# Kernel tuning notes

Measured on AMD Instinct MI355X. Metric: run time of the kernel, lower is better.

## Reference

```python
import jax, jax.numpy as jnp
import numpy as np

N_NODES = 100000
N_EDGES = 1600000
DIMS = [64, 64, 64, 32]  # [n_feat] + hid


def setup_inputs() -> dict:
    key = jax.random.key(0)
    ks = jax.random.split(key, 2 + 2 * (len(DIMS) - 1))
    x = jax.random.normal(ks[0], (N_NODES, DIMS[0]), dtype=jnp.float32)
    edge_index = jax.random.randint(ks[1], (2, N_EDGES), 0, N_NODES, dtype=jnp.int64)
    inp = {"x": x, "edge_index": edge_index}
    for i in range(len(DIMS) - 1):
        fan_in, fan_out = DIMS[i], DIMS[i + 1]
        scale = 1.0 / np.sqrt(fan_in)
        inp[f"W{i+1}"] = jax.random.normal(ks[2 + 2 * i], (fan_in, fan_out), dtype=jnp.float32) * scale
        inp[f"b{i+1}"] = jax.random.normal(ks[3 + 2 * i], (fan_out,), dtype=jnp.float32) * scale
    return inp


def _gcn_conv(x, W, b, src, dst, dis):
    # h = X W ; out[i] = sum_{j->i} norm_ij * h[j] + dis[i]^2 * h[i] + b
    h = x @ W
    norm = dis[src] * dis[dst]                      # [E]
    agg = jax.ops.segment_sum(h[src] * norm[:, None], dst, num_segments=x.shape[0])
    agg = agg + h * (dis * dis)[:, None]            # self-loop contribution
    return agg + b


def reference(x, edge_index, W1, b1, W2, b2, W3, b3):
    src, dst = edge_index[0], edge_index[1]
    n = x.shape[0]
    # degree with self-loops (edge weight 1), symmetric normalization
    deg = jax.ops.segment_sum(jnp.ones(src.shape[0], x.dtype), dst, num_segments=n) + 1.0
    dis = jax.lax.rsqrt(deg)
    h = jax.nn.relu(_gcn_conv(x, W1, b1, src, dst, dis))   # dropout is identity in eval
    h = jax.nn.relu(_gcn_conv(h, W2, b2, src, dst, dis))
    return _gcn_conv(h, W3, b3, src, dst, dis)
```

## Files before the change

kernel.cpp:

```cpp
#include <hip/hip_runtime.h>


typedef __attribute__((ext_vector_type(8))) _Float16 half8;

static inline int cdiv(int a, int b) { return (a + b - 1) / b; }

#define ACHUNK 4096
#define MAXNBK 512

__global__ void k_bucket_hist(const int* __restrict__ dst, int* __restrict__ counts_t,
                              int NBK, int NBA, int E) {
    __shared__ int cnt[MAXNBK];
    int t = threadIdx.x, b = blockIdx.x;
    for (int i = t; i < NBK; i += 256) cnt[i] = 0;
    __syncthreads();
    int e0 = b * ACHUNK;
#pragma unroll
    for (int j = 0; j < ACHUNK / 256; ++j) {
        int e = e0 + j * 256 + t;
        if (e < E) atomicAdd(&cnt[dst[e] >> 8], 1);
    }
    __syncthreads();
    for (int i = t; i < NBK; i += 256) counts_t[i * NBA + b] = cnt[i];
}

#define SCAN_T 256
#define SCAN_V 4
#define SCAN_CHUNK 1024

__global__ void k_scan_partial(const int* __restrict__ a, int* __restrict__ bsum, int n) {
    __shared__ int red[SCAN_T];
    int t = threadIdx.x, b = blockIdx.x;
    int base = b * SCAN_CHUNK + t * SCAN_V;
    int s = 0;
#pragma unroll
    for (int j = 0; j < SCAN_V; ++j) { int i = base + j; if (i < n) s += a[i]; }
    red[t] = s;
    __syncthreads();
    for (int off = SCAN_T / 2; off > 0; off >>= 1) {
        if (t < off) red[t] += red[t + off];
        __syncthreads();
    }
    if (t == 0) bsum[b] = red[0];
}

__global__ void k_scan_bsum(int* bsum, int nb) {
    __shared__ int sh[1024];
    int t = threadIdx.x;
    int v = (t < nb) ? bsum[t] : 0;
    sh[t] = v;
    __syncthreads();
    for (int off = 1; off < 1024; off <<= 1) {
        int u = (t >= off) ? sh[t - off] : 0;
        __syncthreads();
        sh[t] += u;
        __syncthreads();
    }
    if (t < nb) bsum[t] = sh[t] - v;
}

__global__ void k_scan_final(const int* __restrict__ a, const int* __restrict__ bsum,
                             int* __restrict__ out, int n) {
    __shared__ int sh[SCAN_T];
    int t = threadIdx.x, b = blockIdx.x;
    int base = b * SCAN_CHUNK + t * SCAN_V;
    int v[SCAN_V];
    int s = 0;
#pragma unroll
    for (int j = 0; j < SCAN_V; ++j) {
        int i = base + j;
        v[j] = (i < n) ? a[i] : 0;
        s += v[j];
    }
    sh[t] = s;
    __syncthreads();
    for (int off = 1; off < SCAN_T; off <<= 1) {
        int u = (t >= off) ? sh[t - off] : 0;
        __syncthreads();
        sh[t] += u;
        __syncthreads();
    }
    int run = sh[t] - s + bsum[b];
#pragma unroll
    for (int j = 0; j < SCAN_V; ++j) {
        int i = base + j;
        if (i < n) { out[i] = run; run += v[j]; }
    }
}

__global__ void k_bucket_scatter(const int* __restrict__ src, const int* __restrict__ dst,
                                 const int* __restrict__ offsets, unsigned* __restrict__ bucketed,
                                 int NBK, int NBA, int E) {
    __shared__ int curs[MAXNBK];
    int t = threadIdx.x, b = blockIdx.x;
    for (int i = t; i < NBK; i += 256) curs[i] = offsets[i * NBA + b];
    __syncthreads();
    int e0 = b * ACHUNK;
#pragma unroll
    for (int j = 0; j < ACHUNK / 256; ++j) {
        int e = e0 + j * 256 + t;
        if (e < E) {
            int d = dst[e];
            int pos = atomicAdd(&curs[d >> 8], 1);
            bucketed[pos] = (unsigned)src[e] | ((unsigned)(d & 255) << 24);
        }
    }
}

__global__ void k_bucket_build(const unsigned* __restrict__ bucketed,
                               const int* __restrict__ offsets,
                               int* __restrict__ csr_src, int* __restrict__ row_start,
                               float* __restrict__ dis, int NBK, int NBA, int N, int E) {
    __shared__ int cnt[256];
    __shared__ int sc[256];
    int t = threadIdx.x, k = blockIdx.x;
    int base = offsets[k * NBA];
    int end = (k + 1 < NBK) ? offsets[(k + 1) * NBA] : E;
    cnt[t] = 0;
    __syncthreads();
    for (int i = base + t; i < end; i += 256)
        atomicAdd(&cnt[bucketed[i] >> 24], 1);
    __syncthreads();
    int c = cnt[t];
    sc[t] = c;
    __syncthreads();
    for (int off = 1; off < 256; off <<= 1) {
        int u = (t >= off) ? sc[t - off] : 0;
        __syncthreads();
        sc[t] += u;
        __syncthreads();
    }
    int excl = sc[t] - c;
    int node = k * 256 + t;
    if (node < N) {
        row_start[node] = base + excl;
        dis[node] = rsqrtf(1.0f + (float)c);
    }
    if (k == 0 && t == 0) row_start[N] = E;
    cnt[t] = base + excl;
    __syncthreads();
    for (int i = base + t; i < end; i += 256) {
        unsigned w = bucketed[i];
        int pos = atomicAdd(&cnt[w >> 24], 1);
        csr_src[pos] = (int)(w & 0xFFFFFFu);
    }
}

template <int K, int M>
__global__ void k_gemm(const float* __restrict__ X, const float* __restrict__ W,
                       const float* __restrict__ dis, _Float16* __restrict__ H, int n) {
    constexpr int CPT = 8;
    constexpr int TPR = M / CPT;
    constexpr int ROWS = 256 / TPR;
    constexpr int KP = K + 1;
    __shared__ float Ws[K * M];
    __shared__ float Xs[ROWS * KP];
    int tid = threadIdx.x;
    for (int idx = tid; idx < K * M / 4; idx += 256)
        ((float4*)Ws)[idx] = ((const float4*)W)[idx];
    int row0 = blockIdx.x * ROWS;
    for (int idx = tid; idx < ROWS * (K / 4); idx += 256) {
        int r = idx / (K / 4), kq = idx % (K / 4);
        int row = row0 + r;
        float4 vv = (row < n) ? ((const float4*)X)[(size_t)row * (K / 4) + kq]
                              : make_float4(0.f, 0.f, 0.f, 0.f);
        Xs[r * KP + kq * 4 + 0] = vv.x;
        Xs[r * KP + kq * 4 + 1] = vv.y;
        Xs[r * KP + kq * 4 + 2] = vv.z;
        Xs[r * KP + kq * 4 + 3] = vv.w;
    }
    __syncthreads();
    int r = tid / TPR, c0 = (tid % TPR) * CPT;
    int row = row0 + r;
    if (row >= n) return;
    float4 a0 = make_float4(0.f, 0.f, 0.f, 0.f);
    float4 a1 = make_float4(0.f, 0.f, 0.f, 0.f);
#pragma unroll
    for (int k = 0; k < K; ++k) {
        float xv = Xs[r * KP + k];
        float4 w0 = ((const float4*)Ws)[(k * M + c0) / 4];
        float4 w1 = ((const float4*)Ws)[(k * M + c0) / 4 + 1];
        a0.x = fmaf(xv, w0.x, a0.x);
        a0.y = fmaf(xv, w0.y, a0.y);
        a0.z = fmaf(xv, w0.z, a0.z);
        a0.w = fmaf(xv, w0.w, a0.w);
        a1.x = fmaf(xv, w1.x, a1.x);
        a1.y = fmaf(xv, w1.y, a1.y);
        a1.z = fmaf(xv, w1.z, a1.z);
        a1.w = fmaf(xv, w1.w, a1.w);
    }
    float dn = dis[row];
    half8 hv;
    hv[0] = (_Float16)(a0.x * dn);
    hv[1] = (_Float16)(a0.y * dn);
    hv[2] = (_Float16)(a0.z * dn);
    hv[3] = (_Float16)(a0.w * dn);
    hv[4] = (_Float16)(a1.x * dn);
    hv[5] = (_Float16)(a1.y * dn);
    hv[6] = (_Float16)(a1.z * dn);
    hv[7] = (_Float16)(a1.w * dn);
    ((half8*)H)[(size_t)row * (M / CPT) + c0 / CPT] = hv;
}

template <int M, bool RELU>
__global__ void k_aggregate(const _Float16* __restrict__ h, const float* __restrict__ dis,
                            const int* __restrict__ row_start, const int* __restrict__ csr_src,
                            const float* __restrict__ b, float* __restrict__ out, int n) {
    constexpr int G = M / 8;
    constexpr int S = 64 / G;
    int gtid = blockIdx.x * blockDim.x + threadIdx.x;
    int node = gtid >> 6;
    if (node >= n) return;
    int lane = threadIdx.x & 63;
    int fg = lane % G;
    int slot = lane / G;
    int e1 = row_start[node + 1];
    const half8* h8 = (const half8*)h;
    float acc[8];
#pragma unroll
    for (int j = 0; j < 8; ++j) acc[j] = 0.f;
    int e = row_start[node] + slot;
    for (; e + S < e1; e += 2 * S) {
        int s0 = csr_src[e];
        int s1 = csr_src[e + S];
        half8 v0 = h8[(size_t)s0 * G + fg];
        half8 v1 = h8[(size_t)s1 * G + fg];
#pragma unroll
        for (int j = 0; j < 8; ++j) acc[j] += (float)v0[j] + (float)v1[j];
    }
    if (e < e1) {
        int s0 = csr_src[e];
        half8 v0 = h8[(size_t)s0 * G + fg];
#pragma unroll
        for (int j = 0; j < 8; ++j) acc[j] += (float)v0[j];
    }
#pragma unroll
    for (int off = G; off < 64; off <<= 1) {
#pragma unroll
        for (int j = 0; j < 8; ++j) acc[j] += __shfl_xor(acc[j], off, 64);
    }
    if (slot == 0) {
        float dn = dis[node];
        half8 hv = h8[(size_t)node * G + fg];
        const float* bp = b + fg * 8;
        float r[8];
#pragma unroll
        for (int j = 0; j < 8; ++j) {
            r[j] = (acc[j] + (float)hv[j]) * dn + bp[j];
            if (RELU) r[j] = fmaxf(r[j], 0.f);
        }
        float4* op = (float4*)(out + (size_t)node * M + fg * 8);
        op[0] = make_float4(r[0], r[1], r[2], r[3]);
        op[1] = make_float4(r[4], r[5], r[6], r[7]);
    }
}

extern "C" void kernel_launch(void* const* d_in, const int* in_sizes, int n_in,
                              void* d_out, int out_size, void* d_ws, size_t ws_size,
                              hipStream_t stream) {
    const float* x   = (const float*)d_in[0];
    const int*   ei  = (const int*)d_in[1];
    const float* W1  = (const float*)d_in[2];
    const float* b1  = (const float*)d_in[3];
    const float* W2  = (const float*)d_in[4];
    const float* b2  = (const float*)d_in[5];
    const float* W3  = (const float*)d_in[6];
    const float* b3  = (const float*)d_in[7];
    float* out = (float*)d_out;

    const int N = in_sizes[0] / 64;
    const int E = in_sizes[1] / 2;
    const int* src = ei;
    const int* dst = ei + E;

    const int NBK = cdiv(N, 256);
    const int NBA = cdiv(E, ACHUNK);
    const int nmat = NBK * NBA;

    const size_t Np = (size_t)((N + 63) / 64) * 64;
    char* p = (char*)d_ws;
    int*      counts_t = (int*)p;      p += (size_t)nmat * sizeof(int);
    int*      offsets  = (int*)p;      p += (size_t)nmat * sizeof(int);
    int*      bsum     = (int*)p;      p += 1024 * sizeof(int);
    int*      row_start= (int*)p;      p += (Np + 64) * sizeof(int);
    float*    dis      = (float*)p;    p += Np * sizeof(float);
    unsigned* bucketed = (unsigned*)p; p += (size_t)E * sizeof(unsigned);
    int*      csr_src  = (int*)p;      p += (size_t)E * sizeof(int);
    _Float16* bufH     = (_Float16*)p; p += Np * 64 * sizeof(_Float16);
    float*    bufX     = (float*)p;    p += Np * 64 * sizeof(float);
    (void)ws_size;

    const int B = 256;
    const int nb = cdiv(nmat, SCAN_CHUNK);

    k_bucket_hist<<<NBA, B, 0, stream>>>(dst, counts_t, NBK, NBA, E);
    k_scan_partial<<<nb, B, 0, stream>>>(counts_t, bsum, nmat);
    k_scan_bsum<<<1, 1024, 0, stream>>>(bsum, nb);
    k_scan_final<<<nb, B, 0, stream>>>(counts_t, bsum, offsets, nmat);
    k_bucket_scatter<<<NBA, B, 0, stream>>>(src, dst, offsets, bucketed, NBK, NBA, E);
    k_bucket_build<<<NBK, B, 0, stream>>>(bucketed, offsets, csr_src, row_start, dis,
                                          NBK, NBA, N, E);

    k_gemm<64, 64><<<cdiv(N, 32), B, 0, stream>>>(x, W1, dis, bufH, N);
    k_aggregate<64, true><<<cdiv(N * 64, B), B, 0, stream>>>(
        bufH, dis, row_start, csr_src, b1, bufX, N);

    k_gemm<64, 64><<<cdiv(N, 32), B, 0, stream>>>(bufX, W2, dis, bufH, N);
    k_aggregate<64, true><<<cdiv(N * 64, B), B, 0, stream>>>(
        bufH, dis, row_start, csr_src, b2, bufX, N);

    k_gemm<64, 32><<<cdiv(N, 64), B, 0, stream>>>(bufX, W3, dis, bufH, N);
    k_aggregate<32, false><<<cdiv(N * 64, B), B, 0, stream>>>(
        bufH, dis, row_start, csr_src, b3, out, N);
}
```

Before: 335.4 us.

## Remap aggregation to lanes-per-feature-pair, store fp16 intermediates, fuse scan

Aggregation now assigns M/2 lanes per node, with each lane accumulating two features across all edges serially, so multiple nodes share a wave and no shuffle reduction is needed. Inter-layer activations are written as fp16, and a new GEMM variant reads half inputs, halving that traffic. The separate block-sum scan kernel is folded into the final scan, and the edge chunk size is doubled with partial unrolling. The trade-offs are longer serial dependency chains per lane with fewer loads in flight, and added fp16 rounding of the activations.

Result: slower. 369.9 us (+10.3%).

```diff
diff --git a/kernel.cpp b/kernel.cpp
--- a/kernel.cpp
+++ b/kernel.cpp
@@ -2,10 +2,11 @@
 
 
 typedef __attribute__((ext_vector_type(8))) _Float16 half8;
+typedef __attribute__((ext_vector_type(2))) _Float16 h2f;
 
 static inline int cdiv(int a, int b) { return (a + b - 1) / b; }
 
-#define ACHUNK 4096
+#define ACHUNK 8192
 #define MAXNBK 512
 
 __global__ void k_bucket_hist(const int* __restrict__ dst, int* __restrict__ counts_t,
@@ -15,7 +16,7 @@
     for (int i = t; i < NBK; i += 256) cnt[i] = 0;
     __syncthreads();
     int e0 = b * ACHUNK;
-#pragma unroll
+#pragma unroll 8
     for (int j = 0; j < ACHUNK / 256; ++j) {
         int e = e0 + j * 256 + t;
         if (e < E) atomicAdd(&cnt[dst[e] >> 8], 1);
@@ -44,26 +45,21 @@
     if (t == 0) bsum[b] = red[0];
 }
 
-__global__ void k_scan_bsum(int* bsum, int nb) {
-    __shared__ int sh[1024];
-    int t = threadIdx.x;
-    int v = (t < nb) ? bsum[t] : 0;
-    sh[t] = v;
-    __syncthreads();
-    for (int off = 1; off < 1024; off <<= 1) {
-        int u = (t >= off) ? sh[t - off] : 0;
-        __syncthreads();
-        sh[t] += u;
-        __syncthreads();
-    }
-    if (t < nb) bsum[t] = sh[t] - v;
-}
-
 __global__ void k_scan_final(const int* __restrict__ a, const int* __restrict__ bsum,
-                             int* __restrict__ out, int n) {
+                             int* __restrict__ out, int nb, int n) {
+    __shared__ int sb[256];
     __shared__ int sh[SCAN_T];
-    int t = threadIdx.x, b = blockIdx.x;
-    int base = b * SCAN_CHUNK + t * SCAN_V;
+    int t = threadIdx.x, bk = blockIdx.x;
+    sb[t] = (t < nb) ? bsum[t] : 0;
+    __syncthreads();
+    for (int off = 1; off < 256; off <<= 1) {
+        int u = (t >= off) ? sb[t - off] : 0;
+        __syncthreads();
+        sb[t] += u;
+        __syncthreads();
+    }
+    int bbase = (bk == 0) ? 0 : sb[bk - 1];
+    int base = bk * SCAN_CHUNK + t * SCAN_V;
     int v[SCAN_V];
     int s = 0;
 #pragma unroll
@@ -80,7 +76,7 @@
         sh[t] += u;
         __syncthreads();
     }
-    int run = sh[t] - s + bsum[b];
+    int run = sh[t] - s + bbase;
 #pragma unroll
     for (int j = 0; j < SCAN_V; ++j) {
         int i = base + j;
@@ -96,7 +92,7 @@
     for (int i = t; i < NBK; i += 256) curs[i] = offsets[i * NBA + b];
     __syncthreads();
     int e0 = b * ACHUNK;
-#pragma unroll
+#pragma unroll 8
     for (int j = 0; j < ACHUNK / 256; ++j) {
         int e = e0 + j * 256 + t;
         if (e < E) {
@@ -147,10 +143,49 @@
 }
 
 template <int K, int M>
-__global__ void k_gemm(const float* __restrict__ X, const float* __restrict__ W,
-                       const float* __restrict__ dis, _Float16* __restrict__ H, int n) {
+__device__ inline void gemm_core(const float* Ws, const float* Xs,
+                                 const float* __restrict__ dis,
+                                 _Float16* __restrict__ H, int row0, int n) {
     constexpr int CPT = 8;
     constexpr int TPR = M / CPT;
+    constexpr int KP = K + 1;
+    int tid = threadIdx.x;
+    int r = tid / TPR, c0 = (tid % TPR) * CPT;
+    int row = row0 + r;
+    if (row >= n) return;
+    float4 a0 = make_float4(0.f, 0.f, 0.f, 0.f);
+    float4 a1 = make_float4(0.f, 0.f, 0.f, 0.f);
+#pragma unroll
+    for (int k = 0; k < K; ++k) {
+        float xv = Xs[r * KP + k];
+        float4 w0 = ((const float4*)Ws)[(k * M + c0) / 4];
+        float4 w1 = ((const float4*)Ws)[(k * M + c0) / 4 + 1];
+        a0.x = fmaf(xv, w0.x, a0.x);
+        a0.y = fmaf(xv, w0.y, a0.y);
+        a0.z = fmaf(xv, w0.z, a0.z);
+        a0.w = fmaf(xv, w0.w, a0.w);
+        a1.x = fmaf(xv, w1.x, a1.x);
+        a1.y = fmaf(xv, w1.y, a1.y);
+        a1.z = fmaf(xv, w1.z, a1.z);
+        a1.w = fmaf(xv, w1.w, a1.w);
+    }
+    float dn = dis[row];
+    half8 hv;
+    hv[0] = (_Float16)(a0.x * dn);
+    hv[1] = (_Float16)(a0.y * dn);
+    hv[2] = (_Float16)(a0.z * dn);
+    hv[3] = (_Float16)(a0.w * dn);
+    hv[4] = (_Float16)(a1.x * dn);
+    hv[5] = (_Float16)(a1.y * dn);
+    hv[6] = (_Float16)(a1.z * dn);
+    hv[7] = (_Float16)(a1.w * dn);
+    ((half8*)H)[(size_t)row * (M / CPT) + c0 / CPT] = hv;
+}
+
+template <int K, int M>
+__global__ void k_gemm_f(const float* __restrict__ X, const float* __restrict__ W,
+                         const float* __restrict__ dis, _Float16* __restrict__ H, int n) {
+    constexpr int TPR = M / 8;
     constexpr int ROWS = 256 / TPR;
     constexpr int KP = K + 1;
     __shared__ float Ws[K * M];
@@ -170,89 +205,87 @@
         Xs[r * KP + kq * 4 + 3] = vv.w;
     }
     __syncthreads();
-    int r = tid / TPR, c0 = (tid % TPR) * CPT;
-    int row = row0 + r;
-    if (row >= n) return;
-    float4 a0 = make_float4(0.f, 0.f, 0.f, 0.f);
-    float4 a1 = make_float4(0.f, 0.f, 0.f, 0.f);
-#pragma unroll
-    for (int k = 0; k < K; ++k) {
-        float xv = Xs[r * KP + k];
-        float4 w0 = ((const float4*)Ws)[(k * M + c0) / 4];
-        float4 w1 = ((const float4*)Ws)[(k * M + c0) / 4 + 1];
-        a0.x = fmaf(xv, w0.x, a0.x);
-        a0.y = fmaf(xv, w0.y, a0.y);
-        a0.z = fmaf(xv, w0.z, a0.z);
-        a0.w = fmaf(xv, w0.w, a0.w);
-        a1.x = fmaf(xv, w1.x, a1.x);
-        a1.y = fmaf(xv, w1.y, a1.y);
-        a1.z = fmaf(xv, w1.z, a1.z);
-        a1.w = fmaf(xv, w1.w, a1.w);
-    }
-    float dn = dis[row];
-    half8 hv;
-    hv[0] = (_Float16)(a0.x * dn);
-    hv[1] = (_Float16)(a0.y * dn);
-    hv[2] = (_Float16)(a0.z * dn);
-    hv[3] = (_Float16)(a0.w * dn);
-    hv[4] = (_Float16)(a1.x * dn);
-    hv[5] = (_Float16)(a1.y * dn);
-    hv[6] = (_Float16)(a1.z * dn);
-    hv[7] = (_Float16)(a1.w * dn);
-    ((half8*)H)[(size_t)row * (M / CPT) + c0 / CPT] = hv;
-}
-
-template <int M, bool RELU>
+    gemm_core<K, M>(Ws, Xs, dis, H, row0, n);
+}
+
+template <int K, int M>
+__global__ void k_gemm_h(const _Float16* __restrict__ X, const float* __restrict__ W,
+                         const float* __restrict__ dis, _Float16* __restrict__ H, int n) {
+    constexpr int TPR = M / 8;
+    constexpr int ROWS = 256 / TPR;
+    constexpr int KP = K + 1;
+    __shared__ float Ws[K * M];
+    __shared__ float Xs[ROWS * KP];
+    int tid = threadIdx.x;
+    for (int idx = tid; idx < K * M / 4; idx += 256)
+        ((float4*)Ws)[idx] = ((const float4*)W)[idx];
+    int row0 = blockIdx.x * ROWS;
+    for (int idx = tid; idx < ROWS * (K / 8); idx += 256) {
+        int r = idx / (K / 8), kq = idx % (K / 8);
+        int row = row0 + r;
+        if (row < n) {
+            half8 v = ((const half8*)X)[(size_t)row * (K / 8) + kq];
+#pragma unroll
+            for (int j = 0; j < 8; ++j) Xs[r * KP + kq * 8 + j] = (float)v[j];
+        } else {
+#pragma unroll
+            for (int j = 0; j < 8; ++j) Xs[r * KP + kq * 8 + j] = 0.f;
+        }
+    }
+    __syncthreads();
+    gemm_core<K, M>(Ws, Xs, dis, H, row0, n);
+}
+
+__device__ inline void store2(float* out, size_t idx, float rx, float ry) {
+    ((float2*)out)[idx] = make_float2(rx, ry);
+}
+__device__ inline void store2(_Float16* out, size_t idx, float rx, float ry) {
+    h2f v;
+    v[0] = (_Float16)rx;
+    v[1] = (_Float16)ry;
+    ((h2f*)out)[idx] = v;
+}
+
+template <int M, bool RELU, typename OutT>
 __global__ void k_aggregate(const _Float16* __restrict__ h, const float* __restrict__ dis,
                             const int* __restrict__ row_start, const int* __restrict__ csr_src,
-                            const float* __restrict__ b, float* __restrict__ out, int n) {
-    constexpr int G = M / 8;
-    constexpr int S = 64 / G;
+                            const float* __restrict__ b, OutT* __restrict__ out, int n) {
+    constexpr int LPN = M / 2;
+    constexpr int NPW = 64 / LPN;
     int gtid = blockIdx.x * blockDim.x + threadIdx.x;
-    int node = gtid >> 6;
+    int wave = gtid >> 6;
+    int lane = threadIdx.x & 63;
+    int sub = lane / LPN, fl = lane % LPN;
+    int node = wave * NPW + sub;
     if (node >= n) return;
-    int lane = threadIdx.x & 63;
-    int fg = lane % G;
-    int slot = lane / G;
-    int e1 = row_start[node + 1];
-    const half8* h8 = (const half8*)h;
-    float acc[8];
-#pragma unroll
-    for (int j = 0; j < 8; ++j) acc[j] = 0.f;
-    int e = row_start[node] + slot;
-    for (; e + S < e1; e += 2 * S) {
+    int e = row_start[node], e1 = row_start[node + 1];
+    const h2f* h2 = (const h2f*)h;
+    float ax = 0.f, ay = 0.f, cx = 0.f, cy = 0.f;
+    for (; e + 1 < e1; e += 2) {
         int s0 = csr_src[e];
-        int s1 = csr_src[e + S];
-        half8 v0 = h8[(size_t)s0 * G + fg];
-        half8 v1 = h8[(size_t)s1 * G + fg];
-#pragma unroll
-        for (int j = 0; j < 8; ++j) acc[j] += (float)v0[j] + (float)v1[j];
+        int s1 = csr_src[e + 1];
+        h2f v0 = h2[(size_t)s0 * LPN + fl];
+        h2f v1 = h2[(size_t)s1 * LPN + fl];
+        ax += (float)v0[0];
+        ay += (float)v0[1];
+        cx += (float)v1[0];
+        cy += (float)v1[1];
     }
     if (e < e1) {
         int s0 = csr_src[e];
-        half8 v0 = h8[(size_t)s0 * G + fg];
-#pragma unroll
-        for (int j = 0; j < 8; ++j) acc[j] += (float)v0[j];
-    }
-#pragma unroll
-    for (int off = G; off < 64; off <<= 1) {
-#pragma unroll
-        for (int j = 0; j < 8; ++j) acc[j] += __shfl_xor(acc[j], off, 64);
-    }
-    if (slot == 0) {
-        float dn = dis[node];
-        half8 hv = h8[(size_t)node * G + fg];
-        const float* bp = b + fg * 8;
-        float r[8];
-#pragma unroll
-        for (int j = 0; j < 8; ++j) {
-            r[j] = (acc[j] + (float)hv[j]) * dn + bp[j];
-            if (RELU) r[j] = fmaxf(r[j], 0.f);
-        }
-        float4* op = (float4*)(out + (size_t)node * M + fg * 8);
-        op[0] = make_float4(r[0], r[1], r[2], r[3]);
-        op[1] = make_float4(r[4], r[5], r[6], r[7]);
-    }
+        h2f v0 = h2[(size_t)s0 * LPN + fl];
+        ax += (float)v0[0];
+        ay += (float)v0[1];
+    }
+    ax += cx;
+    ay += cy;
+    float dn = dis[node];
+    h2f hv = h2[(size_t)node * LPN + fl];
+    float2 bb = ((const float2*)b)[fl];
+    float rx = (ax + (float)hv[0]) * dn + bb.x;
+    float ry = (ay + (float)hv[1]) * dn + bb.y;
+    if (RELU) { rx = fmaxf(rx, 0.f); ry = fmaxf(ry, 0.f); }
+    store2(out, (size_t)node * LPN + fl, rx, ry);
 }
 
 extern "C" void kernel_launch(void* const* d_in, const int* in_sizes, int n_in,
@@ -287,7 +320,7 @@
     unsigned* bucketed = (unsigned*)p; p += (size_t)E * sizeof(unsigned);
     int*      csr_src  = (int*)p;      p += (size_t)E * sizeof(int);
     _Float16* bufH     = (_Float16*)p; p += Np * 64 * sizeof(_Float16);
-    float*    bufX     = (float*)p;    p += Np * 64 * sizeof(float);
+    _Float16* bufX     = (_Float16*)p; p += Np * 64 * sizeof(_Float16);
     (void)ws_size;
 
     const int B = 256;
@@ -295,21 +328,23 @@
 
     k_bucket_hist<<<NBA, B, 0, stream>>>(dst, counts_t, NBK, NBA, E);
     k_scan_partial<<<nb, B, 0, stream>>>(counts_t, bsum, nmat);
-    k_scan_bsum<<<1, 1024, 0, stream>>>(bsum, nb);
-    k_scan_final<<<nb, B, 0, stream>>>(counts_t, bsum, offsets, nmat);
+    k_scan_final<<<nb, B, 0, stream>>>(counts_t, bsum, offsets, nb, nmat);
     k_bucket_scatter<<<NBA, B, 0, stream>>>(src, dst, offsets, bucketed, NBK, NBA, E);
     k_bucket_build<<<NBK, B, 0, stream>>>(bucketed, offsets, csr_src, row_start, dis,
                                           NBK, NBA, N, E);
 
-    k_gemm<64, 64><<<cdiv(N, 32), B, 0, stream>>>(x, W1, dis, bufH, N);
-    k_aggregate<64, true><<<cdiv(N * 64, B), B, 0, stream>>>(
+    const int blocks_a64 = cdiv(cdiv(N, 2) * 64, B);
+    const int blocks_a32 = cdiv(cdiv(N, 4) * 64, B);
+
+    k_gemm_f<64, 64><<<cdiv(N, 32), B, 0, stream>>>(x, W1, dis, bufH, N);
+    k_aggregate<64, true, _Float16><<<blocks_a64, B, 0, stream>>>(
         bufH, dis, row_start, csr_src, b1, bufX, N);
 
-    k_gemm<64, 64><<<cdiv(N, 32), B, 0, stream>>>(bufX, W2, dis, bufH, N);
-    k_aggregate<64, true><<<cdiv(N * 64, B), B, 0, stream>>>(
+    k_gemm_h<64, 64><<<cdiv(N, 32), B, 0, stream>>>(bufX, W2, dis, bufH, N);
+    k_aggregate<64, true, _Float16><<<blocks_a64, B, 0, stream>>>(
         bufH, dis, row_start, csr_src, b2, bufX, N);
 
-    k_gemm<64, 32><<<cdiv(N, 64), B, 0, stream>>>(bufX, W3, dis, bufH, N);
-    k_aggregate<32, false><<<cdiv(N * 64, B), B, 0, stream>>>(
+    k_gemm_h<64, 32><<<cdiv(N, 64), B, 0, stream>>>(bufX, W3, dis, bufH, N);
+    k_aggregate<32, false, float><<<blocks_a32, B, 0, stream>>>(
         bufH, dis, row_start, csr_src, b3, out, N);
 }
```
